# Kernel tuning notes

Measured on AMD Instinct MI355X. Metric: run time of the kernel, lower is better.

## Reference

```python
import jax, jax.numpy as jnp
import numpy as np
from math import factorial

LMAX = 8
BATCH = 65536


def _cg(j1, m1, j2, m2, j3, m3):
    """Clebsch-Gordan coefficient <j1 m1 j2 m2 | j3 m3> (Racah formula)."""
    if m1 + m2 != m3:
        return 0.0
    if j3 < abs(j1 - j2) or j3 > j1 + j2:
        return 0.0
    f = factorial
    pre = ((2 * j3 + 1) * f(j1 + j2 - j3) * f(j1 - j2 + j3) * f(-j1 + j2 + j3)
           / f(j1 + j2 + j3 + 1)) ** 0.5
    pre *= (f(j1 + m1) * f(j1 - m1) * f(j2 + m2) * f(j2 - m2)
            * f(j3 + m3) * f(j3 - m3)) ** 0.5
    kmin = max(0, j2 - j3 - m1, j1 - j3 + m2)
    kmax = min(j1 + j2 - j3, j1 - m1, j2 + m2)
    s = 0.0
    for k in range(kmin, kmax + 1):
        s += (-1) ** k / (f(k) * f(j1 + j2 - j3 - k) * f(j1 - m1 - k)
                          * f(j2 + m2 - k) * f(j3 - j2 + m1 + k) * f(j3 - j1 - m2 + k))
    return pre * s


def _cg_tensor(l1, l2, lo):
    C = np.zeros((2 * l1 + 1, 2 * l2 + 1, 2 * lo + 1), dtype=np.float32)
    for i, m1 in enumerate(range(-l1, l1 + 1)):
        for j, m2 in enumerate(range(-l2, l2 + 1)):
            M = m1 + m2
            if abs(M) <= lo:
                C[i, j, M + lo] = _cg(l1, m1, l2, m2, lo, M)
    return jnp.asarray(C)


def _build_full_index_map(lmax):
    im = []
    for l1 in range(lmax + 1):
        for l2 in range(l1, lmax + 1):
            for lv in range(abs(l1 - l2), min(l1 + l2, lmax) + 1):
                im.append((l1, l2, lv))
    return im


def _build_cg_power_index_map(lmax):
    if lmax < 2:
        return []
    entries = []
    for l2 in range(2, lmax + 1):
        lo_min = l2 - 1
        lo_max = min(l2 + 1, lmax)
        entries.append((1, l2, lo_min))
        if l2 >= 4 and lo_min + 1 <= lo_max:
            entries.append((1, l2, lo_min + 1))
    for l2 in range(3, lmax + 1):
        lo_min = l2 - 2
        lo_max = min(l2 + 2, lmax)
        entries.append((2, l2, lo_min))
        if lo_min + 1 <= lo_max:
            entries.append((2, l2, lo_min + 1))
    if lmax >= 3:
        entries.append((3, 3, 2))
    for l2 in range(4, lmax + 1):
        lo_min = l2 - 3
        lo_max = min(l2 + 3, lmax)
        entries.append((3, l2, lo_min))
        if l2 % 2 == 1 and l2 >= 5:
            if lo_min + 1 <= lo_max:
                entries.append((3, l2, lo_min + 1))
            if lo_min + 2 <= lo_max:
                entries.append((3, l2, lo_min + 2))
    return entries


FULL_MAP = _build_full_index_map(LMAX)
POWER_MAP = _build_cg_power_index_map(LMAX)
_CG = {t: _cg_tensor(*t) for t in sorted(set(FULL_MAP) | set(POWER_MAP))}
N_OUT = len(FULL_MAP) + len(POWER_MAP)


def setup_inputs() -> dict:
    k1, k2 = jax.random.split(jax.random.key(0))
    shape = (BATCH, LMAX + 1, LMAX + 1)
    return {
        "coeffs_real": jax.random.normal(k1, shape, dtype=jnp.float32),
        "coeffs_imag": jax.random.normal(k2, shape, dtype=jnp.float32),
    }


def _full_coeffs(c):
    """Extend m>=0 coefficients to full m range: F_l^{-m} = (-1)^m conj(F_l^m)."""
    F = {}
    for l in range(LMAX + 1):
        pos = c[:, l, :l + 1]  # (B, l+1), m = 0..l
        if l == 0:
            F[l] = pos
        else:
            signs = jnp.asarray((-1.0) ** np.arange(1, l + 1), dtype=jnp.float32)
            neg = (signs * jnp.conj(pos[:, 1:]))[:, ::-1]  # m = -l..-1
            F[l] = jnp.concatenate([neg, pos], axis=1)  # (B, 2l+1)
    return F


def reference(coeffs_real, coeffs_imag):
    c = (coeffs_real + 1j * coeffs_imag).astype(jnp.complex64)
    F = _full_coeffs(c)
    outs = []
    # scalar bispectrum entries: beta = sum_{m1,m2} C F1 F2 conj(F_lo^{m1+m2})
    for (l1, l2, lo) in FULL_MAP:
        C = _CG[(l1, l2, lo)]
        G = jnp.einsum('bi,bj,ijk->bk', F[l1], F[l2], C)  # coupled component, (B, 2lo+1)
        beta = jnp.sum(G * jnp.conj(F[lo]), axis=1)
        outs.append(beta.real)
    for (l1, l2, lo) in POWER_MAP:
        C = _CG[(l1, l2, lo)]
        G = jnp.einsum('bi,bj,ijk->bk', F[l1], F[l2], C)
        outs.append(jnp.sum(G.real ** 2 + G.imag ** 2, axis=1))
    return jnp.stack(outs, axis=1)  # (B, N_OUT) float32
```

## Files before the change

### kernel.cpp

```cpp
#include <hip/hip_runtime.h>
#include <math.h>
#include <utility>

#define LMAX 8
#define NENT 249
#define EPB 128
#define TPB 256
#define ESTRIDE 130
#define NCO 45
#define PLANE (NCO*ESTRIDE)
#define NRE 289

typedef __attribute__((ext_vector_type(2))) float f32x2;

struct Ent { int l1, l2, lo, ty; };

__host__ __device__ constexpr int tri_(int l){ return l*(l+1)/2; }

__host__ __device__ constexpr Ent ent_of(int want){
  Ent r{0,0,0,0}; int n=0;
  for(int l1=0;l1<=LMAX;l1++)
    for(int l2=l1;l2<=LMAX;l2++){
      int hi=l1+l2; if(hi>LMAX)hi=LMAX;
      for(int lo=l2-l1;lo<=hi;lo++){ if(n==want){ r=Ent{l1,l2,lo,0}; } n++; }
    }
  for(int l2=2;l2<=LMAX;l2++){
    if(n==want) r=Ent{1,l2,l2-1,1}; n++;
    if(l2>=4){ if(n==want) r=Ent{1,l2,l2,1}; n++; }
  }
  for(int l2=3;l2<=LMAX;l2++){
    if(n==want) r=Ent{2,l2,l2-2,1}; n++;
    if(n==want) r=Ent{2,l2,l2-1,1}; n++;
  }
  if(n==want) r=Ent{3,3,2,1}; n++;
  for(int l2=4;l2<=LMAX;l2++){
    if(n==want) r=Ent{3,l2,l2-3,1}; n++;
    if((l2&1)&&l2>=5){
      if(n==want) r=Ent{3,l2,l2-2,1}; n++;
      if(n==want) r=Ent{3,l2,l2-1,1}; n++;
    }
  }
  return r;
}
__host__ __device__ constexpr int ent_count(){
  int n=0;
  for(int l1=0;l1<=LMAX;l1++)
    for(int l2=l1;l2<=LMAX;l2++){
      int hi=l1+l2; if(hi>LMAX)hi=LMAX;
      for(int lo=l2-l1;lo<=hi;lo++) n++;
    }
  for(int l2=2;l2<=LMAX;l2++){ n++; if(l2>=4) n++; }
  for(int l2=3;l2<=LMAX;l2++) n+=2;
  n++;
  for(int l2=4;l2<=LMAX;l2++){ n++; if((l2&1)&&l2>=5) n+=2; }
  return n;
}
static_assert(ent_count()==NENT, "entry count mismatch");

__host__ __device__ constexpr int sr_(int m){ return m>=0 ? 1 : (((-m)&1)? -1 : 1); }
__host__ __device__ constexpr int sq_(int m){ return m>=0 ? 1 : (((-m)&1)? 1 : -1); }

__device__ double cg_(int j1,int m1,int j2,int m2,int j3,int m3){
  if (m1+m2 != m3) return 0.0;
  int dj = j1-j2; if(dj<0) dj=-dj;
  if (j3 < dj || j3 > j1+j2) return 0.0;
  double f[26]; f[0]=1.0;
  for (int t=1;t<26;t++) f[t]=f[t-1]*(double)t;
  double pre = sqrt((2.0*j3+1.0)*f[j1+j2-j3]*f[j1-j2+j3]*f[-j1+j2+j3]/f[j1+j2+j3+1]);
  pre *= sqrt(f[j1+m1]*f[j1-m1]*f[j2+m2]*f[j2-m2]*f[j3+m3]*f[j3-m3]);
  int kmin = 0; if (j2-j3-m1>kmin) kmin=j2-j3-m1; if (j1-j3+m2>kmin) kmin=j1-j3+m2;
  int kmax = j1+j2-j3; if (j1-m1<kmax) kmax=j1-m1; if (j2+m2<kmax) kmax=j2+m2;
  double s=0.0;
  for (int k=kmin;k<=kmax;k++){
    double term = 1.0/(f[k]*f[j1+j2-j3-k]*f[j1-m1-k]*f[j2+m2-k]*f[j3-j2+m1+k]*f[j3-j1-m2+k]);
    s += (k&1)? -term : term;
  }
  return pre*s;
}

__global__ void setup_kernel(float* __restrict__ ws){
  int e = blockIdx.x;
  Ent E = ent_of(e);
  int ni = 2*E.l1+1, nk = 2*E.lo+1, tot = ni*nk;
  int t = threadIdx.x;
  if (t < tot){
    int k = t/ni, i = t - k*ni;
    int m1 = i-E.l1, M = k-E.lo, m2 = M-m1;
    float C = 0.f;
    if (m2>=-E.l2 && m2<=E.l2) C = (float)cg_(E.l1,m1,E.l2,m2,E.lo,M);
    ws[(long long)e*NRE + t] = C;
  }
}

template<int EE>
__device__ __attribute__((always_inline)) inline f32x2 proc_entry(
    const float* __restrict__ lds, const float* __restrict__ rec, int lane2)
{
  constexpr Ent E = ent_of(EE);
  constexpr int L1=E.l1, L2=E.l2, LO=E.lo, TY=E.ty;
  constexpr int NI = 2*L1+1;
  constexpr int B1 = tri_(L1), B2 = tri_(L2), B3 = tri_(LO);

  f32x2 F1r[NI], F1i[NI];
  if constexpr (L1 <= 5){
#pragma unroll
    for (int i=0;i<NI;i++){
      int am = i<L1 ? L1-i : i-L1;
      F1r[i] = *(const f32x2*)&lds[(B1+am)*ESTRIDE + lane2];
      F1i[i] = *(const f32x2*)&lds[PLANE + (B1+am)*ESTRIDE + lane2];
    }
  }

  f32x2 acc = {0.f, 0.f};
#pragma unroll
  for (int k=0;k<=2*LO;k++){
    const int M = k-LO;
    f32x2 Gr = {0.f,0.f}, Gi = {0.f,0.f};
#pragma unroll
    for (int i=0;i<NI;i++){
      const int m1 = i-L1;
      const int m2 = M-m1;
      const int am2 = m2<0? -m2:m2;
      if (am2 <= L2){
        float C = rec[k*NI+i];
        f32x2 c2 = *(const f32x2*)&lds[(B2+am2)*ESTRIDE + lane2];
        f32x2 d2 = *(const f32x2*)&lds[PLANE + (B2+am2)*ESTRIDE + lane2];
        f32x2 a, b;
        if constexpr (L1 <= 5){ a = F1r[i]; b = F1i[i]; }
        else {
          int am1 = m1<0? -m1:m1;
          a = *(const f32x2*)&lds[(B1+am1)*ESTRIDE + lane2];
          b = *(const f32x2*)&lds[PLANE + (B1+am1)*ESTRIDE + lane2];
        }
        const int r1=sr_(m1), q1=sq_(m1), r2=sr_(m2), q2=sq_(m2);
        const int s1=r1*r2, s2=-(q1*q2), s3=r1*q2, s4=q1*r2;
        f32x2 t1 = (s1>0? a : -a) * c2;
        t1 = __builtin_elementwise_fma((s2>0? b : -b), d2, t1);
        f32x2 t2 = (s3>0? a : -a) * d2;
        t2 = __builtin_elementwise_fma((s4>0? b : -b), c2, t2);
        f32x2 Cv = {C, C};
        Gr = __builtin_elementwise_fma(Cv, t1, Gr);
        Gi = __builtin_elementwise_fma(Cv, t2, Gi);
      }
    }
    if constexpr (TY==0){
      const int aM = M<0? -M:M;
      f32x2 xr = *(const f32x2*)&lds[(B3+aM)*ESTRIDE + lane2];
      f32x2 yi = *(const f32x2*)&lds[PLANE + (B3+aM)*ESTRIDE + lane2];
      const int AL = sr_(M), BE = sq_(M);
      acc = __builtin_elementwise_fma(Gr, (AL>0? xr : -xr), acc);
      acc = __builtin_elementwise_fma(Gi, (BE>0? yi : -yi), acc);
    } else {
      acc = __builtin_elementwise_fma(Gr, Gr, acc);
      acc = __builtin_elementwise_fma(Gi, Gi, acc);
    }
  }
  return acc;
}

template<int EE>
__device__ __attribute__((always_inline)) inline void chain_step(
    const float* __restrict__ lds, const float* __restrict__ ws,
    float* __restrict__ out, int lane2, int s, int e_,
    long long baseA, f32x2* obuf)
{
  if (EE >= s && EE < e_){
    obuf[EE & 7] = proc_entry<EE>(lds, ws + (long long)EE*NRE, lane2);
  }
  if constexpr (((EE & 7) == 7) || (EE == NENT-1)){
    constexpr int G8 = EE & ~7;
#pragma unroll
    for (int j=0; j <= (EE&7); j++){
      if (G8+j >= s && G8+j < e_){
        out[baseA + G8 + j]        = obuf[j].x;
        out[baseA + NENT + G8 + j] = obuf[j].y;
      }
    }
  }
}

template<int... Es>
__device__ __attribute__((always_inline)) inline void chain_all(
    std::integer_sequence<int, Es...>,
    const float* __restrict__ lds, const float* __restrict__ ws,
    float* __restrict__ out, int lane2, int s, int e_,
    long long baseA, f32x2* obuf)
{
  (chain_step<Es>(lds, ws, out, lane2, s, e_, baseA, obuf), ...);
}

__global__ __launch_bounds__(TPB, 3) void main_kernel(
    const float* __restrict__ re, const float* __restrict__ im,
    float* __restrict__ out, const float* __restrict__ ws, int4 bnd)
{
  __shared__ float lds[2*PLANE];
  const int gbase = blockIdx.x*EPB;
  for (int t=threadIdx.x; t<EPB*81; t+=TPB){
    float vr = re[(size_t)gbase*81 + t];
    float vi = im[(size_t)gbase*81 + t];
    int elem = t/81, x = t - elem*81;
    int l = x/9, m = x - l*9;
    if (m<=l){
      int off = tri_(l)+m;
      lds[off*ESTRIDE+elem] = vr;
      lds[PLANE + off*ESTRIDE+elem] = vi;
    }
  }
  __syncthreads();

  const int lane  = threadIdx.x & 63;
  const int wv    = __builtin_amdgcn_readfirstlane(threadIdx.x >> 6);
  const int lane2 = lane*2;
  const int s  = (wv==0)? 0     : (wv==1)? bnd.x : (wv==2)? bnd.y : bnd.z;
  const int e_ = (wv==0)? bnd.x : (wv==1)? bnd.y : (wv==2)? bnd.z : bnd.w;
  const long long baseA = (long long)(gbase + lane2)*NENT;

  f32x2 obuf[8];
#pragma unroll
  for (int j=0;j<8;j++) obuf[j] = f32x2{0.f,0.f};

  chain_all(std::make_integer_sequence<int, NENT>{},
            lds, ws, out, lane2, s, e_, baseA, obuf);
}

extern "C" void kernel_launch(void* const* d_in, const int* in_sizes, int n_in,
                              void* d_out, int out_size, void* d_ws, size_t ws_size,
                              hipStream_t stream) {
  const float* re = (const float*)d_in[0];
  const float* im = (const float*)d_in[1];
  float* out = (float*)d_out;
  float* ws  = (float*)d_ws;
  const int batch = in_sizes[0] / 81;

  double w[NENT], tot = 0.0;
  for (int e=0;e<NENT;e++){
    Ent E = ent_of(e);
    w[e] = (double)((2*E.l1+1)*(2*E.lo+1) + 2*(2*E.lo+1));
    tot += w[e];
  }
  int ends[4]; double acc = 0.0; int c = 0;
  for (int e=0;e<NENT && c<3;e++){
    acc += w[e];
    if (acc >= tot*(c+1)/4.0){ ends[c++] = e+1; }
  }
  while (c<3) ends[c++] = NENT;
  ends[3] = NENT;
  int4 bnd = make_int4(ends[0], ends[1], ends[2], ends[3]);

  setup_kernel<<<NENT, 320, 0, stream>>>(ws);
  main_kernel<<<batch/EPB, TPB, 0, stream>>>(re, im, out, ws, bnd);
}
```

Measured before the change: 430.1 us.

## Group entries by (l1,l2) pair, share products, constexpr CG tables, stage output in LDS

```diff
diff --git a/kernel.cpp b/kernel.cpp
--- a/kernel.cpp
+++ b/kernel.cpp
@@ -1,200 +1,230 @@
 #include <hip/hip_runtime.h>
-#include <math.h>
 #include <utility>
 
 #define LMAX 8
 #define NENT 249
+#define NPAIR 45
 #define EPB 128
-#define TPB 256
-#define ESTRIDE 130
+#define TPB 512
+#define ESTR 130
 #define NCO 45
-#define PLANE (NCO*ESTRIDE)
-#define NRE 289
+#define PLANE (NCO*ESTR)
+#define P1END 30
+#define FSPLIT 100
+#define PSLOT 115
+#define NSLOT 149
 
 typedef __attribute__((ext_vector_type(2))) float f32x2;
 
-struct Ent { int l1, l2, lo, ty; };
+struct P2 { int l1, l2; };
 
 __host__ __device__ constexpr int tri_(int l){ return l*(l+1)/2; }
-
-__host__ __device__ constexpr Ent ent_of(int want){
-  Ent r{0,0,0,0}; int n=0;
-  for(int l1=0;l1<=LMAX;l1++)
-    for(int l2=l1;l2<=LMAX;l2++){
-      int hi=l1+l2; if(hi>LMAX)hi=LMAX;
-      for(int lo=l2-l1;lo<=hi;lo++){ if(n==want){ r=Ent{l1,l2,lo,0}; } n++; }
-    }
-  for(int l2=2;l2<=LMAX;l2++){
-    if(n==want) r=Ent{1,l2,l2-1,1}; n++;
-    if(l2>=4){ if(n==want) r=Ent{1,l2,l2,1}; n++; }
-  }
-  for(int l2=3;l2<=LMAX;l2++){
-    if(n==want) r=Ent{2,l2,l2-2,1}; n++;
-    if(n==want) r=Ent{2,l2,l2-1,1}; n++;
-  }
-  if(n==want) r=Ent{3,3,2,1}; n++;
-  for(int l2=4;l2<=LMAX;l2++){
-    if(n==want) r=Ent{3,l2,l2-3,1}; n++;
-    if((l2&1)&&l2>=5){
-      if(n==want) r=Ent{3,l2,l2-2,1}; n++;
-      if(n==want) r=Ent{3,l2,l2-1,1}; n++;
-    }
-  }
-  return r;
-}
-__host__ __device__ constexpr int ent_count(){
-  int n=0;
-  for(int l1=0;l1<=LMAX;l1++)
-    for(int l2=l1;l2<=LMAX;l2++){
-      int hi=l1+l2; if(hi>LMAX)hi=LMAX;
-      for(int lo=l2-l1;lo<=hi;lo++) n++;
-    }
-  for(int l2=2;l2<=LMAX;l2++){ n++; if(l2>=4) n++; }
-  for(int l2=3;l2<=LMAX;l2++) n+=2;
-  n++;
-  for(int l2=4;l2<=LMAX;l2++){ n++; if((l2&1)&&l2>=5) n+=2; }
-  return n;
-}
-static_assert(ent_count()==NENT, "entry count mismatch");
-
 __host__ __device__ constexpr int sr_(int m){ return m>=0 ? 1 : (((-m)&1)? -1 : 1); }
 __host__ __device__ constexpr int sq_(int m){ return m>=0 ? 1 : (((-m)&1)? 1 : -1); }
 
-__device__ double cg_(int j1,int m1,int j2,int m2,int j3,int m3){
+__host__ __device__ constexpr P2 pair_of(int w){
+  int n=0;
+  for(int a=0;a<=LMAX;a++) for(int b=a;b<=LMAX;b++){ if(n==w) return P2{a,b}; n++; }
+  return P2{0,0};
+}
+
+__host__ __device__ constexpr int full_rank(int l1,int l2,int lo){
+  int r=0;
+  for(int a=0;a<=LMAX;a++) for(int b=a;b<=LMAX;b++){
+    int hi=a+b>LMAX?LMAX:a+b;
+    for(int c=b-a;c<=hi;c++){ if(a==l1&&b==l2&&c==lo) return r; r++; }
+  }
+  return -1;
+}
+
+__host__ __device__ constexpr int power_idx(int l1,int l2,int lo){
+  int n=0;
+  for(int b=2;b<=LMAX;b++){
+    if(l1==1&&l2==b&&lo==b-1) return n; n++;
+    if(b>=4){ if(l1==1&&l2==b&&lo==b) return n; n++; }
+  }
+  for(int b=3;b<=LMAX;b++){
+    if(l1==2&&l2==b&&lo==b-2) return n; n++;
+    if(l1==2&&l2==b&&lo==b-1) return n; n++;
+  }
+  if(l1==3&&l2==3&&lo==2) return n; n++;
+  for(int b=4;b<=LMAX;b++){
+    if(l1==3&&l2==b&&lo==b-3) return n; n++;
+    if((b&1)&&b>=5){
+      if(l1==3&&l2==b&&lo==b-2) return n; n++;
+      if(l1==3&&l2==b&&lo==b-1) return n; n++;
+    }
+  }
+  return -1;
+}
+
+__host__ __device__ constexpr double csqrt_(double x){
+  if (x<=0.0) return 0.0;
+  double v=x, s=1.0;
+  while (v>4.0){ v*=0.25; s*=2.0; }
+  while (v<0.25){ v*=4.0; s*=0.5; }
+  double g=v;
+  for(int i=0;i<48;i++) g=0.5*(g+v/g);
+  return g*s;
+}
+__host__ __device__ constexpr double cgC(int j1,int m1,int j2,int m2,int j3,int m3){
   if (m1+m2 != m3) return 0.0;
-  int dj = j1-j2; if(dj<0) dj=-dj;
-  if (j3 < dj || j3 > j1+j2) return 0.0;
-  double f[26]; f[0]=1.0;
-  for (int t=1;t<26;t++) f[t]=f[t-1]*(double)t;
-  double pre = sqrt((2.0*j3+1.0)*f[j1+j2-j3]*f[j1-j2+j3]*f[-j1+j2+j3]/f[j1+j2+j3+1]);
-  pre *= sqrt(f[j1+m1]*f[j1-m1]*f[j2+m2]*f[j2-m2]*f[j3+m3]*f[j3-m3]);
-  int kmin = 0; if (j2-j3-m1>kmin) kmin=j2-j3-m1; if (j1-j3+m2>kmin) kmin=j1-j3+m2;
-  int kmax = j1+j2-j3; if (j1-m1<kmax) kmax=j1-m1; if (j2+m2<kmax) kmax=j2+m2;
+  int dj=j1-j2; if(dj<0)dj=-dj;
+  if (j3<dj || j3>j1+j2) return 0.0;
+  if (m2<-j2 || m2>j2 || m1<-j1 || m1>j1 || m3<-j3 || m3>j3) return 0.0;
+  double f[26]={}; f[0]=1.0;
+  for(int t=1;t<26;t++) f[t]=f[t-1]*(double)t;
+  double pre = csqrt_((2.0*j3+1.0)*f[j1+j2-j3]*f[j1-j2+j3]*f[-j1+j2+j3]/f[j1+j2+j3+1]);
+  pre *= csqrt_(f[j1+m1]*f[j1-m1]*f[j2+m2]*f[j2-m2]*f[j3+m3]*f[j3-m3]);
+  int kmin=0; if(j2-j3-m1>kmin)kmin=j2-j3-m1; if(j1-j3+m2>kmin)kmin=j1-j3+m2;
+  int kmax=j1+j2-j3; if(j1-m1<kmax)kmax=j1-m1; if(j2+m2<kmax)kmax=j2+m2;
   double s=0.0;
-  for (int k=kmin;k<=kmax;k++){
+  for(int k=kmin;k<=kmax;k++){
     double term = 1.0/(f[k]*f[j1+j2-j3-k]*f[j1-m1-k]*f[j2+m2-k]*f[j3-j2+m1+k]*f[j3-j1-m2+k]);
     s += (k&1)? -term : term;
   }
   return pre*s;
 }
 
-__global__ void setup_kernel(float* __restrict__ ws){
-  int e = blockIdx.x;
-  Ent E = ent_of(e);
-  int ni = 2*E.l1+1, nk = 2*E.lo+1, tot = ni*nk;
-  int t = threadIdx.x;
-  if (t < tot){
-    int k = t/ni, i = t - k*ni;
-    int m1 = i-E.l1, M = k-E.lo, m2 = M-m1;
-    float C = 0.f;
-    if (m2>=-E.l2 && m2<=E.l2) C = (float)cg_(E.l1,m1,E.l2,m2,E.lo,M);
-    ws[(long long)e*NRE + t] = C;
-  }
-}
-
-template<int EE>
-__device__ __attribute__((always_inline)) inline f32x2 proc_entry(
-    const float* __restrict__ lds, const float* __restrict__ rec, int lane2)
+template<int L1,int L2>
+struct CGTab {
+  static constexpr int LOmx = (L1+L2<LMAX)?(L1+L2):LMAX;
+  static constexpr int LOmn = L2-L1;
+  static constexpr int NLO  = LOmx-LOmn+1;
+  float c[NLO][2*LOmx+1][2*L1+1];
+};
+template<int L1,int L2>
+__host__ __device__ constexpr CGTab<L1,L2> make_cgtab(){
+  CGTab<L1,L2> T{};
+  for(int lo=T.LOmn; lo<=T.LOmx; lo++)
+    for(int M=-T.LOmx; M<=T.LOmx; M++)
+      for(int m1=-L1;m1<=L1;m1++){
+        double v=0.0;
+        if (M>=-lo && M<=lo){
+          int m2=M-m1;
+          if(m2>=-L2&&m2<=L2) v = cgC(L1,m1,L2,m2,lo,M);
+        }
+        T.c[lo-T.LOmn][M+T.LOmx][m1+L1] = (float)v;
+      }
+  return T;
+}
+
+template<int PI>
+__device__ __attribute__((always_inline)) inline void do_pair(
+    const float* __restrict__ lds, float* __restrict__ stage, int lane2)
 {
-  constexpr Ent E = ent_of(EE);
-  constexpr int L1=E.l1, L2=E.l2, LO=E.lo, TY=E.ty;
-  constexpr int NI = 2*L1+1;
-  constexpr int B1 = tri_(L1), B2 = tri_(L2), B3 = tri_(LO);
-
-  f32x2 F1r[NI], F1i[NI];
-  if constexpr (L1 <= 5){
-#pragma unroll
-    for (int i=0;i<NI;i++){
-      int am = i<L1 ? L1-i : i-L1;
-      F1r[i] = *(const f32x2*)&lds[(B1+am)*ESTRIDE + lane2];
-      F1i[i] = *(const f32x2*)&lds[PLANE + (B1+am)*ESTRIDE + lane2];
-    }
-  }
-
-  f32x2 acc = {0.f, 0.f};
-#pragma unroll
-  for (int k=0;k<=2*LO;k++){
-    const int M = k-LO;
-    f32x2 Gr = {0.f,0.f}, Gi = {0.f,0.f};
-#pragma unroll
-    for (int i=0;i<NI;i++){
-      const int m1 = i-L1;
+  constexpr P2 pe = pair_of(PI);
+  constexpr int L1 = pe.l1, L2 = pe.l2;
+  constexpr int LOmin = L2-L1;
+  constexpr int LOmax = (L1+L2<LMAX)?(L1+L2):LMAX;
+  constexpr int NLO = LOmax-LOmin+1;
+  constexpr int B1 = tri_(L1), B2 = tri_(L2);
+  constexpr auto tab = make_cgtab<L1,L2>();
+
+  f32x2 X1[L1+1], Y1[L1+1], X2[L2+1], Y2[L2+1];
+#pragma unroll
+  for (int a=0;a<=L1;a++){
+    X1[a] = *(const f32x2*)&lds[(B1+a)*ESTR + lane2];
+    Y1[a] = *(const f32x2*)&lds[PLANE + (B1+a)*ESTR + lane2];
+  }
+#pragma unroll
+  for (int a=0;a<=L2;a++){
+    X2[a] = *(const f32x2*)&lds[(B2+a)*ESTR + lane2];
+    Y2[a] = *(const f32x2*)&lds[PLANE + (B2+a)*ESTR + lane2];
+  }
+
+  f32x2 bAcc[NLO], pAcc[NLO];
+#pragma unroll
+  for (int t=0;t<NLO;t++){ bAcc[t]=f32x2{0.f,0.f}; pAcc[t]=f32x2{0.f,0.f}; }
+
+#pragma unroll
+  for (int M=-LOmax; M<=LOmax; M++){
+    const int m1lo = (M-L2 > -L1) ? (M-L2) : -L1;
+    const int m1hi = (M+L2 <  L1) ? (M+L2) :  L1;
+    f32x2 Prd[2*L1+1], Pid[2*L1+1];
+#pragma unroll
+    for (int m1=-L1; m1<=L1; m1++){
+      if (m1<m1lo || m1>m1hi) continue;
+      const int i  = m1-m1lo;
       const int m2 = M-m1;
-      const int am2 = m2<0? -m2:m2;
-      if (am2 <= L2){
-        float C = rec[k*NI+i];
-        f32x2 c2 = *(const f32x2*)&lds[(B2+am2)*ESTRIDE + lane2];
-        f32x2 d2 = *(const f32x2*)&lds[PLANE + (B2+am2)*ESTRIDE + lane2];
-        f32x2 a, b;
-        if constexpr (L1 <= 5){ a = F1r[i]; b = F1i[i]; }
-        else {
-          int am1 = m1<0? -m1:m1;
-          a = *(const f32x2*)&lds[(B1+am1)*ESTRIDE + lane2];
-          b = *(const f32x2*)&lds[PLANE + (B1+am1)*ESTRIDE + lane2];
+      const int a1 = m1<0?-m1:m1, a2 = m2<0?-m2:m2;
+      const int s1 = sr_(m1)*sr_(m2);
+      const int s2 = -(sq_(m1)*sq_(m2));
+      const int s3 = sr_(m1)*sq_(m2);
+      const int s4 = sq_(m1)*sr_(m2);
+      f32x2 t1 = (s1>0? X1[a1] : -X1[a1]) * X2[a2];
+      Prd[i] = __builtin_elementwise_fma((s2>0? Y1[a1] : -Y1[a1]), Y2[a2], t1);
+      f32x2 t2 = (s3>0? X1[a1] : -X1[a1]) * Y2[a2];
+      Pid[i] = __builtin_elementwise_fma((s4>0? Y1[a1] : -Y1[a1]), X2[a2], t2);
+    }
+#pragma unroll
+    for (int lo=LOmin; lo<=LOmax; lo++){
+      if (lo < (M<0?-M:M)) continue;
+      f32x2 Gr = {0.f,0.f}, Gi = {0.f,0.f};
+#pragma unroll
+      for (int m1=-L1; m1<=L1; m1++){
+        if (m1<m1lo || m1>m1hi) continue;
+        const int i = m1-m1lo;
+        const float C = tab.c[lo-LOmin][M+LOmax][m1+L1];
+        if (C != 0.f){
+          f32x2 Cv = {C,C};
+          Gr = __builtin_elementwise_fma(Cv, Prd[i], Gr);
+          Gi = __builtin_elementwise_fma(Cv, Pid[i], Gi);
         }
-        const int r1=sr_(m1), q1=sq_(m1), r2=sr_(m2), q2=sq_(m2);
-        const int s1=r1*r2, s2=-(q1*q2), s3=r1*q2, s4=q1*r2;
-        f32x2 t1 = (s1>0? a : -a) * c2;
-        t1 = __builtin_elementwise_fma((s2>0? b : -b), d2, t1);
-        f32x2 t2 = (s3>0? a : -a) * d2;
-        t2 = __builtin_elementwise_fma((s4>0? b : -b), c2, t2);
-        f32x2 Cv = {C, C};
-        Gr = __builtin_elementwise_fma(Cv, t1, Gr);
-        Gi = __builtin_elementwise_fma(Cv, t2, Gi);
       }
-    }
-    if constexpr (TY==0){
-      const int aM = M<0? -M:M;
-      f32x2 xr = *(const f32x2*)&lds[(B3+aM)*ESTRIDE + lane2];
-      f32x2 yi = *(const f32x2*)&lds[PLANE + (B3+aM)*ESTRIDE + lane2];
+      const int aM = M<0?-M:M;
+      const int B3 = tri_(lo);
+      f32x2 x3 = *(const f32x2*)&lds[(B3+aM)*ESTR + lane2];
+      f32x2 y3 = *(const f32x2*)&lds[PLANE + (B3+aM)*ESTR + lane2];
       const int AL = sr_(M), BE = sq_(M);
-      acc = __builtin_elementwise_fma(Gr, (AL>0? xr : -xr), acc);
-      acc = __builtin_elementwise_fma(Gi, (BE>0? yi : -yi), acc);
-    } else {
-      acc = __builtin_elementwise_fma(Gr, Gr, acc);
-      acc = __builtin_elementwise_fma(Gi, Gi, acc);
-    }
-  }
-  return acc;
-}
-
-template<int EE>
-__device__ __attribute__((always_inline)) inline void chain_step(
-    const float* __restrict__ lds, const float* __restrict__ ws,
-    float* __restrict__ out, int lane2, int s, int e_,
-    long long baseA, f32x2* obuf)
+      bAcc[lo-LOmin] = __builtin_elementwise_fma(Gr, (AL>0? x3 : -x3), bAcc[lo-LOmin]);
+      bAcc[lo-LOmin] = __builtin_elementwise_fma(Gi, (BE>0? y3 : -y3), bAcc[lo-LOmin]);
+      if (power_idx(L1,L2,lo) >= 0){
+        pAcc[lo-LOmin] = __builtin_elementwise_fma(Gr, Gr, pAcc[lo-LOmin]);
+        pAcc[lo-LOmin] = __builtin_elementwise_fma(Gi, Gi, pAcc[lo-LOmin]);
+      }
+    }
+  }
+
+#pragma unroll
+  for (int lo=LOmin; lo<=LOmax; lo++){
+    const int fr   = full_rank(L1,L2,lo);
+    const int slot = fr<FSPLIT ? fr : fr-FSPLIT;
+    *(f32x2*)&stage[slot*ESTR + lane2] = bAcc[lo-LOmin];
+    const int pidx = power_idx(L1,L2,lo);
+    if (pidx>=0)
+      *(f32x2*)&stage[(PSLOT+pidx)*ESTR + lane2] = pAcc[lo-LOmin];
+  }
+}
+
+template<int PI>
+__device__ __attribute__((always_inline)) inline void pair_step(
+    const float* __restrict__ lds, float* __restrict__ stage, int lane2, int s, int e_)
 {
-  if (EE >= s && EE < e_){
-    obuf[EE & 7] = proc_entry<EE>(lds, ws + (long long)EE*NRE, lane2);
-  }
-  if constexpr (((EE & 7) == 7) || (EE == NENT-1)){
-    constexpr int G8 = EE & ~7;
-#pragma unroll
-    for (int j=0; j <= (EE&7); j++){
-      if (G8+j >= s && G8+j < e_){
-        out[baseA + G8 + j]        = obuf[j].x;
-        out[baseA + NENT + G8 + j] = obuf[j].y;
-      }
-    }
-  }
-}
-
-template<int... Es>
-__device__ __attribute__((always_inline)) inline void chain_all(
-    std::integer_sequence<int, Es...>,
-    const float* __restrict__ lds, const float* __restrict__ ws,
-    float* __restrict__ out, int lane2, int s, int e_,
-    long long baseA, f32x2* obuf)
+  if (PI>=s && PI<e_) do_pair<PI>(lds, stage, lane2);
+}
+template<int OFF, int... Ps>
+__device__ __attribute__((always_inline)) inline void pair_range(
+    std::integer_sequence<int,Ps...>,
+    const float* __restrict__ lds, float* __restrict__ stage, int lane2, int s, int e_)
 {
-  (chain_step<Es>(lds, ws, out, lane2, s, e_, baseA, obuf), ...);
-}
-
-__global__ __launch_bounds__(TPB, 3) void main_kernel(
+  (pair_step<OFF+Ps>(lds, stage, lane2, s, e_), ...);
+}
+
+struct Bnd { int e1[8]; int e2[8]; };
+
+constexpr int LDS_FLOATS = 2*PLANE + NSLOT*ESTR;
+constexpr int LDS_BYTES  = LDS_FLOATS*4;
+static_assert(LDS_BYTES <= 160*1024, "LDS over 160KB");
+
+__global__ __launch_bounds__(TPB, 2) void main_kernel(
     const float* __restrict__ re, const float* __restrict__ im,
-    float* __restrict__ out, const float* __restrict__ ws, int4 bnd)
+    float* __restrict__ out, Bnd bnd)
 {
-  __shared__ float lds[2*PLANE];
+  extern __shared__ float lds[];
+  float* stage = lds + 2*PLANE;
   const int gbase = blockIdx.x*EPB;
+
   for (int t=threadIdx.x; t<EPB*81; t+=TPB){
     float vr = re[(size_t)gbase*81 + t];
     float vi = im[(size_t)gbase*81 + t];
@@ -202,8 +232,8 @@
     int l = x/9, m = x - l*9;
     if (m<=l){
       int off = tri_(l)+m;
-      lds[off*ESTRIDE+elem] = vr;
-      lds[PLANE + off*ESTRIDE+elem] = vi;
+      lds[off*ESTR+elem] = vr;
+      lds[PLANE + off*ESTR+elem] = vi;
     }
   }
   __syncthreads();
@@ -211,16 +241,28 @@
   const int lane  = threadIdx.x & 63;
   const int wv    = __builtin_amdgcn_readfirstlane(threadIdx.x >> 6);
   const int lane2 = lane*2;
-  const int s  = (wv==0)? 0     : (wv==1)? bnd.x : (wv==2)? bnd.y : bnd.z;
-  const int e_ = (wv==0)? bnd.x : (wv==1)? bnd.y : (wv==2)? bnd.z : bnd.w;
-  const long long baseA = (long long)(gbase + lane2)*NENT;
-
-  f32x2 obuf[8];
-#pragma unroll
-  for (int j=0;j<8;j++) obuf[j] = f32x2{0.f,0.f};
-
-  chain_all(std::make_integer_sequence<int, NENT>{},
-            lds, ws, out, lane2, s, e_, baseA, obuf);
+  const int s1 = (wv==0)? 0      : bnd.e1[wv-1];
+  const int E1 = bnd.e1[wv];
+  const int s2 = (wv==0)? P1END  : bnd.e2[wv-1];
+  const int E2 = bnd.e2[wv];
+  const long long obase = (long long)gbase*NENT;
+
+  pair_range<0>(std::make_integer_sequence<int,P1END>{}, lds, stage, lane2, s1, E1);
+  __syncthreads();
+
+  for (int p=threadIdx.x; p<EPB*FSPLIT; p+=TPB){
+    int elem = p/FSPLIT, o = p - elem*FSPLIT;
+    out[obase + (long long)elem*NENT + o] = stage[o*ESTR + elem];
+  }
+  __syncthreads();
+
+  pair_range<P1END>(std::make_integer_sequence<int,NPAIR-P1END>{}, lds, stage, lane2, s2, E2);
+  __syncthreads();
+
+  for (int p=threadIdx.x; p<EPB*NSLOT; p+=TPB){
+    int elem = p/NSLOT, o = p - elem*NSLOT;
+    out[obase + (long long)elem*NENT + FSPLIT + o] = stage[o*ESTR + elem];
+  }
 }
 
 extern "C" void kernel_launch(void* const* d_in, const int* in_sizes, int n_in,
@@ -229,24 +271,42 @@
   const float* re = (const float*)d_in[0];
   const float* im = (const float*)d_in[1];
   float* out = (float*)d_out;
-  float* ws  = (float*)d_ws;
   const int batch = in_sizes[0] / 81;
 
-  double w[NENT], tot = 0.0;
-  for (int e=0;e<NENT;e++){
-    Ent E = ent_of(e);
-    w[e] = (double)((2*E.l1+1)*(2*E.lo+1) + 2*(2*E.lo+1));
-    tot += w[e];
-  }
-  int ends[4]; double acc = 0.0; int c = 0;
-  for (int e=0;e<NENT && c<3;e++){
-    acc += w[e];
-    if (acc >= tot*(c+1)/4.0){ ends[c++] = e+1; }
-  }
-  while (c<3) ends[c++] = NENT;
-  ends[3] = NENT;
-  int4 bnd = make_int4(ends[0], ends[1], ends[2], ends[3]);
-
-  setup_kernel<<<NENT, 320, 0, stream>>>(ws);
-  main_kernel<<<batch/EPB, TPB, 0, stream>>>(re, im, out, ws, bnd);
-}
+  hipFuncSetAttribute((const void*)main_kernel,
+                      hipFuncAttributeMaxDynamicSharedMemorySize, LDS_BYTES);
+
+  double w[NPAIR];
+  for (int p=0;p<NPAIR;p++){
+    P2 pe = pair_of(p);
+    int L1=pe.l1, L2=pe.l2;
+    int LOmx=(L1+L2<LMAX)?(L1+L2):LMAX, LOmn=L2-L1;
+    double ww = 2.0*(L1+L2+2);
+    for (int M=-LOmx;M<=LOmx;M++){
+      int lo_ = (M-L2>-L1)?(M-L2):-L1, hi_ = (M+L2<L1)?(M+L2):L1;
+      int dn = hi_-lo_+1;
+      ww += 4.0*dn;
+      int aM = M<0?-M:M;
+      for (int lo=(LOmn>aM?LOmn:aM); lo<=LOmx; lo++)
+        ww += 2.0*dn + 2.0 + (power_idx(L1,L2,lo)>=0 ? 2.0 : 0.0);
+    }
+    w[p]=ww;
+  }
+  Bnd bnd;
+  {
+    double tot=0; for(int p=0;p<P1END;p++) tot+=w[p];
+    double acc=0; int c=0;
+    for(int p=0;p<P1END && c<7;p++){ acc+=w[p]; if(acc>=tot*(c+1)/8.0) bnd.e1[c++]=p+1; }
+    while(c<7) bnd.e1[c++]=P1END;
+    bnd.e1[7]=P1END;
+  }
+  {
+    double tot=0; for(int p=P1END;p<NPAIR;p++) tot+=w[p];
+    double acc=0; int c=0;
+    for(int p=P1END;p<NPAIR && c<7;p++){ acc+=w[p]; if(acc>=tot*(c+1)/8.0) bnd.e2[c++]=p+1; }
+    while(c<7) bnd.e2[c++]=NPAIR;
+    bnd.e2[7]=NPAIR;
+  }
+
+  main_kernel<<<batch/EPB, TPB, LDS_BYTES, stream>>>(re, im, out, bnd);
+}
```

After: 368.9 us. 14.2% less time.
